# Kernel tuning notes

Hardware: AMD Instinct MI355X
Metric: run time of the kernel (lower is better)

Reference implementation:

```python
import jax, jax.numpy as jnp
import numpy as np
from jax import lax

DIM = 1024
HEADS = 16
KERNEL = 7
STRIDE = 4
EPS = 1e-5


def setup_inputs() -> dict:
    key = jax.random.key(0)
    ks = jax.random.split(key, 4)
    B, N = 2, 4096
    w_scale = 0.02
    return {
        "x": jax.random.normal(ks[0], (B, N, DIM), dtype=jnp.float32),
        "ln_w": jnp.ones((DIM,), jnp.float32),
        "ln_b": jnp.zeros((DIM,), jnp.float32),
        "Wk": jax.random.normal(ks[1], (DIM, DIM, KERNEL), dtype=jnp.float32) * w_scale,
        "Wv": jax.random.normal(ks[2], (DIM, DIM, KERNEL), dtype=jnp.float32) * w_scale,
        "Wq": jax.random.normal(ks[3], (DIM, DIM, KERNEL), dtype=jnp.float32) * w_scale,
    }


def _conv1d(x_bnd, w):
    # x: (B, N, D) -> conv over sequence dim with 'same' padding; w: (out_ch, in_ch, K)
    x_cn = jnp.transpose(x_bnd, (0, 2, 1))  # (B, D, N)
    pad = KERNEL // 2
    y = lax.conv_general_dilated(
        x_cn, w, window_strides=(1,), padding=[(pad, pad)],
        dimension_numbers=("NCH", "OIH", "NCH"))
    return jnp.transpose(y, (0, 2, 1))  # (B, N, D)


def reference(x, ln_w, ln_b, Wk, Wv, Wq):
    B, N, D = x.shape
    hd = D // HEADS
    # LayerNorm (biased variance, as in torch)
    mu = jnp.mean(x, axis=-1, keepdims=True)
    var = jnp.mean(jnp.square(x - mu), axis=-1, keepdims=True)
    x_n = (x - mu) / jnp.sqrt(var + EPS) * ln_w + ln_b

    K = _conv1d(x_n, Wk)                 # (B, N, D)
    V = _conv1d(x_n, Wv)                 # (B, N, D)
    Q = _conv1d(x_n, Wq)[:, ::STRIDE]    # (B, M, D) windowed queries
    M = Q.shape[1]

    Qh = Q.reshape(B, M, HEADS, hd).transpose(0, 2, 1, 3)  # (B, H, M, hd)
    Kh = K.reshape(B, N, HEADS, hd).transpose(0, 2, 1, 3)  # (B, H, N, hd)
    Vh = V.reshape(B, N, HEADS, hd).transpose(0, 2, 1, 3)  # (B, H, N, hd)

    scale = jnp.sqrt(jnp.asarray(hd, x.dtype))
    scores = jnp.einsum("bhmd,bhnd->bhmn", Qh, Kh) / scale  # (B, H, M, N)
    attn = jax.nn.softmax(scores, axis=-1)
    out = jnp.einsum("bhmn,bhnd->bhmd", attn, Vh)           # (B, H, M, hd)
    out = out.transpose(0, 2, 1, 3).reshape(B, M, D)
    return out + Q
```

## Files before the change

kernel.cpp:

```cpp
#include <hip/hip_runtime.h>

typedef __attribute__((ext_vector_type(4))) float f32x4;
typedef __attribute__((ext_vector_type(8))) short short8;
typedef __attribute__((ext_vector_type(4))) unsigned short u16x4;

#define AS1 __attribute__((address_space(1)))
#define AS3 __attribute__((address_space(3)))

__device__ __forceinline__ unsigned short f2bf(float f) {
  unsigned u = __float_as_uint(f);
  return (unsigned short)((u + 0x7FFFu + ((u >> 16) & 1u)) >> 16);
}
__device__ __forceinline__ unsigned short f2bf_fast(float f) {
  return (unsigned short)((__float_as_uint(f) + 0x8000u) >> 16);
}

__global__ __launch_bounds__(256) void ln_kernel(
    const float* __restrict__ x, const float* __restrict__ lw,
    const float* __restrict__ lb, unsigned short* __restrict__ xpad) {
  __shared__ float red[8];
  int row = blockIdx.x;
  int b = row >> 12, n = row & 4095;
  const float* xr = x + (size_t)row * 1024;
  int c = threadIdx.x * 4;
  f32x4 v = *(const f32x4*)(xr + c);
  float s = v[0] + v[1] + v[2] + v[3];
  float sq = v[0]*v[0] + v[1]*v[1] + v[2]*v[2] + v[3]*v[3];
#pragma unroll
  for (int off = 32; off; off >>= 1) {
    s  += __shfl_xor(s, off, 64);
    sq += __shfl_xor(sq, off, 64);
  }
  int w = threadIdx.x >> 6;
  if ((threadIdx.x & 63) == 0) { red[w*2] = s; red[w*2+1] = sq; }
  __syncthreads();
  float S  = red[0]+red[2]+red[4]+red[6];
  float SQ = red[1]+red[3]+red[5]+red[7];
  float mean = S * (1.0f/1024.0f);
  float var  = SQ * (1.0f/1024.0f) - mean*mean;
  float rstd = rsqrtf(var + 1e-5f);
  f32x4 wv = *(const f32x4*)(lw + c);
  f32x4 bv = *(const f32x4*)(lb + c);
  u16x4 o;
#pragma unroll
  for (int r = 0; r < 4; ++r) o[r] = f2bf((v[r]-mean)*rstd*wv[r] + bv[r]);
  *(u16x4*)(xpad + (((size_t)(b*4102 + n + 3)) << 10) + c) = o;
}

__global__ __launch_bounds__(256) void repack_kernel(
    const float* __restrict__ Wk, const float* __restrict__ Wv,
    const float* __restrict__ Wq, unsigned short* __restrict__ Wt) {
  __shared__ unsigned short t[7168];
  const float* W = (blockIdx.y == 0) ? Wk : (blockIdx.y == 1) ? Wv : Wq;
  int o = blockIdx.x;
  const float* row = W + (size_t)o * 7168;
  unsigned short* orow = Wt + ((size_t)(blockIdx.y * 1024 + o)) * 7168;
#pragma unroll
  for (int p = 0; p < 7; ++p) {
    int idx = p*1024 + threadIdx.x*4;
    f32x4 v = *(const f32x4*)(row + idx);
#pragma unroll
    for (int e = 0; e < 4; ++e) {
      unsigned j = idx + e;
      unsigned i = (j * 149797u) >> 20;
      unsigned k = j - i*7;
      t[k*1024 + i] = f2bf(v[e]);
    }
  }
  __syncthreads();
#pragma unroll
  for (int p = 0; p < 7; ++p) {
    int idx = p*1024 + threadIdx.x*4;
    *(u16x4*)(orow + idx) = *(const u16x4*)(t + idx);
  }
}

__global__ __launch_bounds__(512, 2) void conv256(
    const unsigned short* __restrict__ Apad,
    const unsigned short* __restrict__ Wt,
    unsigned short* __restrict__ Ksg, unsigned short* __restrict__ Vsg,
    float* __restrict__ Qp) {
  __shared__ unsigned short As[2][2][8192];
  __shared__ unsigned short Bs[2][2][8192];

  const int tid = threadIdx.x;
  const int w = tid >> 6, l = tid & 63;
  const int wm = w >> 2, wn = w & 3;
  const int l15 = l & 15, lh4 = l >> 4, l7 = l & 7;
  const int chA = ((l7 & 4) | (lh4 ^ (l7 & 3))) << 3;
  const int wOff = w << 9;
  const int bid = blockIdx.x;
  const int xcd = bid & 7, j = bid >> 3;
  const int ct = j & 7, rt = (xcd << 2) | (j >> 3);

  unsigned aOff[2][2], bOff[2][2];
#pragma unroll
  for (int i = 0; i < 2; ++i) {
    const int idx = i * 512 + tid;
    const int r = idx >> 3;
    const int clog8 = (((idx & 7) ^ (r & 7)) << 3);
#pragma unroll
    for (int hh = 0; hh < 2; ++hh) {
      const int rg = (rt << 8) + (hh << 7) + r;
      aOff[hh][i] = ((unsigned)((rg >> 12) * 4102 + (rg & 4095)) << 10) + clog8;
      const int cg = (ct << 8) + (hh << 7) + r;
      bOff[hh][i] = (unsigned)cg * 7168u + clog8;
    }
  }

  unsigned aRd[4], bRd[2];
#pragma unroll
  for (int fm = 0; fm < 4; ++fm)
    aRd[fm] = (unsigned)(((wm << 6) + (fm << 4) + l15) << 6) + chA;
#pragma unroll
  for (int fn = 0; fn < 2; ++fn)
    bRd[fn] = (unsigned)(((wn << 5) + (fn << 4) + l15) << 6) + chA;

  f32x4 acc[2][2][4][2] = {};
  short8 af[4][2], bfr[2][2];

#define STGA(BUF, HALF, T) do { \
    __builtin_amdgcn_global_load_lds((const AS1 void*)(Apad + aOff[HALF][0] + ((unsigned)(T) << 6)), (AS3 void*)&As[BUF][HALF][wOff], 16, 0, 0); \
    __builtin_amdgcn_global_load_lds((const AS1 void*)(Apad + aOff[HALF][1] + ((unsigned)(T) << 6)), (AS3 void*)&As[BUF][HALF][4096 + wOff], 16, 0, 0); \
  } while (0)
#define STGB(BUF, HALF, T) do { \
    __builtin_amdgcn_global_load_lds((const AS1 void*)(Wt + bOff[HALF][0] + ((unsigned)(T) << 6)), (AS3 void*)&Bs[BUF][HALF][wOff], 16, 0, 0); \
    __builtin_amdgcn_global_load_lds((const AS1 void*)(Wt + bOff[HALF][1] + ((unsigned)(T) << 6)), (AS3 void*)&Bs[BUF][HALF][4096 + wOff], 16, 0, 0); \
  } while (0)
#define LDA(BUF, MQ) do { \
    _Pragma("unroll") for (int fm = 0; fm < 4; ++fm) { \
      af[fm][0] = *(const short8*)&As[BUF][MQ][aRd[fm]]; \
      af[fm][1] = *(const short8*)&As[BUF][MQ][aRd[fm] ^ 32u]; } \
  } while (0)
#define LDB(BUF, NQ) do { \
    _Pragma("unroll") for (int fn = 0; fn < 2; ++fn) { \
      bfr[fn][0] = *(const short8*)&Bs[BUF][NQ][bRd[fn]]; \
      bfr[fn][1] = *(const short8*)&Bs[BUF][NQ][bRd[fn] ^ 32u]; } \
  } while (0)
#define MM(MQ, NQ) do { \
    _Pragma("unroll") for (int ks = 0; ks < 2; ++ks) \
    _Pragma("unroll") for (int fm = 0; fm < 4; ++fm) \
    _Pragma("unroll") for (int fn = 0; fn < 2; ++fn) \
      acc[MQ][NQ][fm][fn] = __builtin_amdgcn_mfma_f32_16x16x32_bf16(af[fm][ks], bfr[fn][ks], acc[MQ][NQ][fm][fn], 0, 0, 0); \
  } while (0)
#define BAR __builtin_amdgcn_s_barrier()
#define LGKM0 asm volatile("s_waitcnt lgkmcnt(0)" ::: "memory")
#define VM6 asm volatile("s_waitcnt vmcnt(6)" ::: "memory")
#define VM0 asm volatile("s_waitcnt vmcnt(0)" ::: "memory")
#define P1 __builtin_amdgcn_s_setprio(1)
#define P0 __builtin_amdgcn_s_setprio(0)

#define RUN_GEMM(NIT) do { \
    STGA(0, 0, 0); STGB(0, 0, 0); STGA(0, 1, 0); STGB(0, 1, 0); \
    STGA(1, 0, 1); STGB(1, 1, 1); STGA(1, 1, 1); \
    VM6; BAR; \
    for (int I = 0; I < (NIT) - 1; ++I) { \
      const int t0 = I * 2; \
      LDA(0, 0); LDB(0, 0); STGB(1, 0, t0 + 1); \
      BAR; LGKM0; P1; MM(0, 0); P0; BAR; \
      LDB(0, 1);            STGA(0, 0, t0 + 2); \
      BAR; LGKM0; P1; MM(0, 1); P0; BAR; \
      LDA(0, 1);            STGB(0, 1, t0 + 2); \
      BAR; LGKM0; P1; MM(1, 1); P0; BAR; \
      LDB(0, 0);            STGA(0, 1, t0 + 2); \
      BAR; LGKM0; P1; MM(1, 0); P0; VM6; BAR; \
      LDA(1, 0); LDB(1, 0); STGB(0, 0, t0 + 2); \
      BAR; LGKM0; P1; MM(0, 0); P0; BAR; \
      LDB(1, 1);            STGA(1, 0, t0 + 3); \
      BAR; LGKM0; P1; MM(0, 1); P0; BAR; \
      LDA(1, 1);            STGB(1, 1, t0 + 3); \
      BAR; LGKM0; P1; MM(1, 1); P0; BAR; \
      LDB(1, 0);            STGA(1, 1, t0 + 3); \
      BAR; LGKM0; P1; MM(1, 0); P0; VM6; BAR; \
    } \
    { \
      LDA(0, 0); LDB(0, 0); STGB(1, 0, ((NIT) - 1) * 2 + 1); \
      BAR; LGKM0; P1; MM(0, 0); P0; BAR; \
      LDB(0, 1); BAR; LGKM0; P1; MM(0, 1); P0; BAR; \
      LDA(0, 1); BAR; LGKM0; P1; MM(1, 1); P0; BAR; \
      LDB(0, 0); BAR; LGKM0; P1; MM(1, 0); P0; VM0; BAR; \
      LDA(1, 0); LDB(1, 0); BAR; LGKM0; P1; MM(0, 0); P0; BAR; \
      LDB(1, 1); BAR; LGKM0; P1; MM(0, 1); P0; BAR; \
      LDA(1, 1); BAR; LGKM0; P1; MM(1, 1); P0; BAR; \
      LDB(1, 0); BAR; LGKM0; P1; MM(1, 0); P0; BAR; \
    } \
  } while (0)

  RUN_GEMM(56);

  if (ct < 4) {
#pragma unroll
    for (int mq = 0; mq < 2; ++mq)
#pragma unroll
      for (int nq = 0; nq < 2; ++nq) {
        const int h = (ct << 2) + (nq << 1) + (wn >> 1);
        const int kd = wn & 1;
#pragma unroll
        for (int fm = 0; fm < 4; ++fm) {
          const int rbase = (rt << 8) + (mq << 7) + (wm << 6) + (fm << 4) + (lh4 << 2);
          const int b = rbase >> 12, n0 = rbase & 4095;
          const size_t base = ((((size_t)((b * 16 + h) * 2 + kd)) << 12) + n0) << 5;
#pragma unroll
          for (int fn = 0; fn < 2; ++fn) {
            const int d32 = (fn << 4) + l15;
#pragma unroll
            for (int rr = 0; rr < 4; ++rr)
              Ksg[base + ((size_t)rr << 5) + d32] = f2bf(acc[mq][nq][fm][fn][rr]);
          }
        }
      }
  } else {
#pragma unroll
    for (int mq = 0; mq < 2; ++mq)
#pragma unroll
      for (int nq = 0; nq < 2; ++nq) {
        const int h = ((ct - 4) << 2) + (nq << 1) + (wn >> 1);
        const int dhi = (wn & 1) << 5;
#pragma unroll
        for (int fm = 0; fm < 4; ++fm) {
          const int rbase = (rt << 8) + (mq << 7) + (wm << 6) + (fm << 4) + (lh4 << 2);
          const int b = rbase >> 12, n = rbase & 4095;
#pragma unroll
          for (int fn = 0; fn < 2; ++fn) {
            const int d = dhi + (fn << 4) + l15;
            const size_t rowbase =
                ((((((size_t)(b * 16 + h)) << 7) + (n >> 5)) << 6) + d) * 32 + (n & 31);
            u16x4 pv;
#pragma unroll
            for (int rr = 0; rr < 4; ++rr) pv[rr] = f2bf(acc[mq][nq][fm][fn][rr]);
            *(u16x4*)(Vsg + rowbase) = pv;
          }
        }
      }
  }

  const int qct = j & 3, qrt = j >> 2, kc = xcd;
  const unsigned kbase = (unsigned)kc * 896u;
#pragma unroll
  for (int i = 0; i < 2; ++i) {
    const int idx = i * 512 + tid;
    const int r = idx >> 3;
    const int clog8 = (((idx & 7) ^ (r & 7)) << 3);
#pragma unroll
    for (int hh = 0; hh < 2; ++hh) {
      const int rg = (qrt << 8) + (hh << 7) + r;
      aOff[hh][i] = ((unsigned)((rg >> 10) * 4102 + ((rg & 1023) << 2)) << 10) + clog8 + kbase;
      const int cg = 2048 + (qct << 8) + (hh << 7) + r;
      bOff[hh][i] = (unsigned)cg * 7168u + clog8 + kbase;
    }
  }
#pragma unroll
  for (int mq = 0; mq < 2; ++mq)
#pragma unroll
    for (int nq = 0; nq < 2; ++nq)
#pragma unroll
      for (int fm = 0; fm < 4; ++fm)
#pragma unroll
        for (int fn = 0; fn < 2; ++fn)
          acc[mq][nq][fm][fn] = (f32x4){0.f, 0.f, 0.f, 0.f};

  RUN_GEMM(7);

  float* Qc = Qp + ((size_t)kc << 21);
#pragma unroll
  for (int mq = 0; mq < 2; ++mq)
#pragma unroll
    for (int nq = 0; nq < 2; ++nq)
#pragma unroll
      for (int fm = 0; fm < 4; ++fm) {
        const int rq = (qrt << 8) + (mq << 7) + (wm << 6) + (fm << 4) + (lh4 << 2);
#pragma unroll
        for (int fn = 0; fn < 2; ++fn) {
          const int cq = (qct << 8) + (nq << 7) + (wn << 5) + (fn << 4) + l15;
#pragma unroll
          for (int rr = 0; rr < 4; ++rr)
            Qc[(((size_t)(rq + rr)) << 10) + cq] = acc[mq][nq][fm][fn][rr];
        }
      }
#undef STGA
#undef STGB
#undef LDA
#undef LDB
#undef MM
#undef BAR
#undef LGKM0
#undef VM6
#undef VM0
#undef P1
#undef P0
#undef RUN_GEMM
}

__global__ __launch_bounds__(256) void qfinal(
    const float* __restrict__ Qp, float* __restrict__ Qf,
    unsigned short* __restrict__ Qsg) {
  const int rq = blockIdx.x;
  const int b = rq >> 10, m = rq & 1023;
  const int c = threadIdx.x << 2;
  f32x4 v = {0.f, 0.f, 0.f, 0.f};
#pragma unroll
  for (int kc = 0; kc < 8; ++kc) {
    f32x4 p = *(const f32x4*)(Qp + ((size_t)kc << 21) + ((size_t)rq << 10) + c);
    v[0] += p[0]; v[1] += p[1]; v[2] += p[2]; v[3] += p[3];
  }
  *(f32x4*)(Qf + ((size_t)rq << 10) + c) = v;
  const int h = c >> 6, kd = (c >> 5) & 1, d32 = c & 31;
  u16x4 o;
#pragma unroll
  for (int e = 0; e < 4; ++e) o[e] = f2bf(v[e]);
  *(u16x4*)(Qsg + ((((size_t)((b * 16 + h) * 2 + kd)) << 10) + m) * 32 + d32) = o;
}

__global__ __launch_bounds__(512) void attn_kernel(
    const unsigned short* __restrict__ Ksg, const unsigned short* __restrict__ Vsg,
    const unsigned short* __restrict__ Qsg, const float* __restrict__ Qf,
    float* __restrict__ out) {
  __shared__ unsigned short Ks[2][8192];
  __shared__ unsigned short Vs[2][8192];
  __shared__ unsigned short Qs[8192];
  __shared__ unsigned short Ps[17408];
  const int tid = threadIdx.x, w = tid >> 6, l = tid & 63;
  const int g = blockIdx.x;
  const int bh = (g & 7) + (((g >> 3) & 3) << 3);
  const int qt = g >> 5;
  const int b = bh >> 4, h = bh & 15;
  const int m0 = qt << 7;
  const int quad = l >> 4, lc = l & 15, l3 = l & 3;
  const float C = 0.18033688011112042f;
  const int lsw = (l & 60) | ((l ^ (l >> 2)) & 3);

  const unsigned short* KgT = Ksg + ((size_t)bh << 18);
  const unsigned short* VgT = Vsg + ((size_t)bh << 18);
  const unsigned short* QgT = Qsg + ((size_t)bh << 16);

#pragma unroll
  for (int p = 0; p < 2; ++p) {
    int t = (w << 1) + p;
    int kd = t >> 3, ml = (t & 7) << 4;
    __builtin_amdgcn_global_load_lds(
        (const AS1 void*)(QgT + ((size_t)((kd << 10) + m0 + ml) << 5) + lsw*8),
        (AS3 void*)(Qs + (t << 9)), 16, 0, 0);
  }

#define STAGE_KV(BUF, N0) do { \
    _Pragma("unroll") for (int p = 0; p < 2; ++p) { \
      int t = (w << 1) + p; \
      __builtin_amdgcn_global_load_lds( \
          (const AS1 void*)(KgT + ((size_t)(((t >> 3) << 12) + (N0) + ((t & 7) << 4)) << 5) + lsw*8), \
          (AS3 void*)(Ks[BUF] + (t << 9)), 16, 0, 0); \
      __builtin_amdgcn_global_load_lds( \
          (const AS1 void*)(VgT + ((size_t)(((((N0) >> 5) + (t >> 2)) << 6) + ((t & 3) << 4)) << 5) + lsw*8), \
          (AS3 void*)(Vs[BUF] + (t << 9)), 16, 0, 0); \
    } \
  } while (0)

  float l_run = 0.f;
  f32x4 oacc[4] = {};
  unsigned short* Pw = Ps + w*2176;

  STAGE_KV(0, 0);
  asm volatile("s_waitcnt vmcnt(0)" ::: "memory");
  __builtin_amdgcn_s_barrier();

  for (int it = 0; it < 32; ++it) {
    const int cur = it & 1;
    if (it < 31) STAGE_KV(cur ^ 1, (it + 1) << 7);
    const unsigned short* Kc = Ks[cur];
    const unsigned short* Vc = Vs[cur];

    const int ch = (quad ^ l3) << 3;
    short8 ak[8][2];
#pragma unroll
    for (int k = 0; k < 2; ++k)
#pragma unroll
      for (int ni = 0; ni < 8; ++ni)
        ak[ni][k] = *(const short8*)(Kc + (k << 12) + ((ni<<4) + lc)*32 + ch);

    f32x4 sv[8] = {};
#pragma unroll
    for (int k = 0; k < 2; ++k) {
      short8 bq = *(const short8*)(Qs + (k << 12) + ((w<<4) + lc)*32 + ch);
#pragma unroll
      for (int ni = 0; ni < 8; ++ni)
        sv[ni] = __builtin_amdgcn_mfma_f32_16x16x32_bf16(ak[ni][k], bq, sv[ni], 0, 0, 0);
    }

    float su = 0.f;
#pragma unroll
    for (int ni = 0; ni < 8; ++ni) {
      u16x4 pv;
#pragma unroll
      for (int rr = 0; rr < 4; ++rr) {
        float pp = __builtin_amdgcn_exp2f(sv[ni][rr] * C);
        su += pp;
        pv[rr] = f2bf_fast(pp);
      }
      *(u16x4*)(Pw + lc*136 + (ni<<4) + (quad<<2)) = pv;
    }
    su += __shfl_xor(su, 16, 64);
    su += __shfl_xor(su, 32, 64);
    l_run += su;

#pragma unroll
    for (int kn = 0; kn < 4; ++kn) {
      short8 bp = *(const short8*)(Pw + lc*136 + (kn<<5) + (quad<<3));
#pragma unroll
      for (int dt = 0; dt < 4; ++dt) {
        short8 av = *(const short8*)(Vc + (kn << 11) + ((dt<<4) + lc)*32 + ch);
        oacc[dt] = __builtin_amdgcn_mfma_f32_16x16x32_bf16(av, bp, oacc[dt], 0, 0, 0);
      }
    }

    asm volatile("s_waitcnt vmcnt(0)" ::: "memory");
    __builtin_amdgcn_s_barrier();
  }
#undef STAGE_KV

  float invl = 1.0f / l_run;
  int m = m0 + (w<<4) + lc;
#pragma unroll
  for (int dt = 0; dt < 4; ++dt) {
    int d = (dt<<4) + (quad<<2);
    size_t off = (((size_t)(b << 10) + m) << 10) + (h << 6) + d;
    f32x4 qv = *(const f32x4*)(Qf + off);
    f32x4 ov;
#pragma unroll
    for (int rr = 0; rr < 4; ++rr) ov[rr] = oacc[dt][rr]*invl + qv[rr];
    *(f32x4*)(out + off) = ov;
  }
}

extern "C" void kernel_launch(void* const* d_in, const int* in_sizes, int n_in,
                              void* d_out, int out_size, void* d_ws, size_t ws_size,
                              hipStream_t stream) {
  const float* x  = (const float*)d_in[0];
  const float* lw = (const float*)d_in[1];
  const float* lb = (const float*)d_in[2];
  const float* Wk = (const float*)d_in[3];
  const float* Wv = (const float*)d_in[4];
  const float* Wq = (const float*)d_in[5];
  float* out = (float*)d_out;

  char* ws = (char*)d_ws;
  size_t off = 0;
  unsigned short* xpad = (unsigned short*)(ws + off); off += (size_t)2*4102*1024*2;
  unsigned short* Wt   = (unsigned short*)(ws + off); off += (size_t)3072*7168*2;
  unsigned short* Ksg  = (unsigned short*)(ws + off); off += (size_t)32*2*4096*32*2;
  unsigned short* Vsg  = (unsigned short*)(ws + off); off += (size_t)32*128*64*32*2;
  unsigned short* Qsg  = (unsigned short*)(ws + off); off += (size_t)32*2*1024*32*2;
  float*          Qf   = (float*)(ws + off);          off += (size_t)2048*1024*4;
  float*          Qp   = (float*)(ws + off);          off += (size_t)8*2048*1024*4;

  for (int b = 0; b < 2; ++b) {
    hipMemsetAsync(xpad + (size_t)b*4102*1024, 0, 3*1024*2, stream);
    hipMemsetAsync(xpad + ((size_t)b*4102 + 4099)*1024, 0, 3*1024*2, stream);
  }
  ln_kernel<<<dim3(8192), dim3(256), 0, stream>>>(x, lw, lb, xpad);
  repack_kernel<<<dim3(1024, 3), dim3(256), 0, stream>>>(Wk, Wv, Wq, Wt);
  conv256<<<dim3(256), dim3(512), 0, stream>>>(xpad, Wt, Ksg, Vsg, Qp);
  qfinal<<<dim3(2048), dim3(256), 0, stream>>>(Qp, Qf, Qsg);
  attn_kernel<<<dim3(256), dim3(512), 0, stream>>>(Ksg, Vsg, Qsg, Qf, out);
}
```

Before: 479.8 us.

## Double-buffer MFMA register fragments to overlap LDS reads with matrix math

The main conv-GEMM loop now keeps two register slots for the A and B fragments. The LDS reads for the next sub-tile are issued before the MFMAs of the current one, so each phase uses one barrier instead of two. The wait counts on the global-to-LDS loads are retuned to vmcnt(4), and the order of the initial staging loads is swapped to match. This is meant to hide LDS read latency and barrier cost behind MFMA work, at the price of more VGPRs and some risk of races from the fewer barriers.

```diff
diff --git a/kernel.cpp b/kernel.cpp
--- a/kernel.cpp
+++ b/kernel.cpp
@@ -117,7 +117,7 @@
     bRd[fn] = (unsigned)(((wn << 5) + (fn << 4) + l15) << 6) + chA;
 
   f32x4 acc[2][2][4][2] = {};
-  short8 af[4][2], bfr[2][2];
+  short8 afS[2][4][2], bfS[2][2][2];
 
 #define STGA(BUF, HALF, T) do { \
     __builtin_amdgcn_global_load_lds((const AS1 void*)(Apad + aOff[HALF][0] + ((unsigned)(T) << 6)), (AS3 void*)&As[BUF][HALF][wOff], 16, 0, 0); \
@@ -127,62 +127,55 @@
     __builtin_amdgcn_global_load_lds((const AS1 void*)(Wt + bOff[HALF][0] + ((unsigned)(T) << 6)), (AS3 void*)&Bs[BUF][HALF][wOff], 16, 0, 0); \
     __builtin_amdgcn_global_load_lds((const AS1 void*)(Wt + bOff[HALF][1] + ((unsigned)(T) << 6)), (AS3 void*)&Bs[BUF][HALF][4096 + wOff], 16, 0, 0); \
   } while (0)
-#define LDA(BUF, MQ) do { \
+#define LDAs(S, BUF, MQ) do { \
     _Pragma("unroll") for (int fm = 0; fm < 4; ++fm) { \
-      af[fm][0] = *(const short8*)&As[BUF][MQ][aRd[fm]]; \
-      af[fm][1] = *(const short8*)&As[BUF][MQ][aRd[fm] ^ 32u]; } \
-  } while (0)
-#define LDB(BUF, NQ) do { \
+      afS[S][fm][0] = *(const short8*)&As[BUF][MQ][aRd[fm]]; \
+      afS[S][fm][1] = *(const short8*)&As[BUF][MQ][aRd[fm] ^ 32u]; } \
+  } while (0)
+#define LDBs(S, BUF, NQ) do { \
     _Pragma("unroll") for (int fn = 0; fn < 2; ++fn) { \
-      bfr[fn][0] = *(const short8*)&Bs[BUF][NQ][bRd[fn]]; \
-      bfr[fn][1] = *(const short8*)&Bs[BUF][NQ][bRd[fn] ^ 32u]; } \
-  } while (0)
-#define MM(MQ, NQ) do { \
+      bfS[S][fn][0] = *(const short8*)&Bs[BUF][NQ][bRd[fn]]; \
+      bfS[S][fn][1] = *(const short8*)&Bs[BUF][NQ][bRd[fn] ^ 32u]; } \
+  } while (0)
+#define MMs(SA, SB, MQ, NQ) do { \
     _Pragma("unroll") for (int ks = 0; ks < 2; ++ks) \
     _Pragma("unroll") for (int fm = 0; fm < 4; ++fm) \
     _Pragma("unroll") for (int fn = 0; fn < 2; ++fn) \
-      acc[MQ][NQ][fm][fn] = __builtin_amdgcn_mfma_f32_16x16x32_bf16(af[fm][ks], bfr[fn][ks], acc[MQ][NQ][fm][fn], 0, 0, 0); \
+      acc[MQ][NQ][fm][fn] = __builtin_amdgcn_mfma_f32_16x16x32_bf16(afS[SA][fm][ks], bfS[SB][fn][ks], acc[MQ][NQ][fm][fn], 0, 0, 0); \
   } while (0)
 #define BAR __builtin_amdgcn_s_barrier()
 #define LGKM0 asm volatile("s_waitcnt lgkmcnt(0)" ::: "memory")
 #define VM6 asm volatile("s_waitcnt vmcnt(6)" ::: "memory")
+#define VM4 asm volatile("s_waitcnt vmcnt(4)" ::: "memory")
 #define VM0 asm volatile("s_waitcnt vmcnt(0)" ::: "memory")
 #define P1 __builtin_amdgcn_s_setprio(1)
 #define P0 __builtin_amdgcn_s_setprio(0)
 
 #define RUN_GEMM(NIT) do { \
-    STGA(0, 0, 0); STGB(0, 0, 0); STGA(0, 1, 0); STGB(0, 1, 0); \
+    STGA(0, 0, 0); STGB(0, 0, 0); STGB(0, 1, 0); STGA(0, 1, 0); \
     STGA(1, 0, 1); STGB(1, 1, 1); STGA(1, 1, 1); \
     VM6; BAR; \
+    LDAs(0, 0, 0); LDBs(0, 0, 0); \
     for (int I = 0; I < (NIT) - 1; ++I) { \
       const int t0 = I * 2; \
-      LDA(0, 0); LDB(0, 0); STGB(1, 0, t0 + 1); \
-      BAR; LGKM0; P1; MM(0, 0); P0; BAR; \
-      LDB(0, 1);            STGA(0, 0, t0 + 2); \
-      BAR; LGKM0; P1; MM(0, 1); P0; BAR; \
-      LDA(0, 1);            STGB(0, 1, t0 + 2); \
-      BAR; LGKM0; P1; MM(1, 1); P0; BAR; \
-      LDB(0, 0);            STGA(0, 1, t0 + 2); \
-      BAR; LGKM0; P1; MM(1, 0); P0; VM6; BAR; \
-      LDA(1, 0); LDB(1, 0); STGB(0, 0, t0 + 2); \
-      BAR; LGKM0; P1; MM(0, 0); P0; BAR; \
-      LDB(1, 1);            STGA(1, 0, t0 + 3); \
-      BAR; LGKM0; P1; MM(0, 1); P0; BAR; \
-      LDA(1, 1);            STGB(1, 1, t0 + 3); \
-      BAR; LGKM0; P1; MM(1, 1); P0; BAR; \
-      LDB(1, 0);            STGA(1, 1, t0 + 3); \
-      BAR; LGKM0; P1; MM(1, 0); P0; VM6; BAR; \
+      BAR; LGKM0; LDBs(1, 0, 1);                STGB(1, 0, t0 + 1); P1; MMs(0, 0, 0, 0); P0; \
+      BAR; LGKM0; LDAs(1, 0, 1);                STGA(0, 0, t0 + 2); P1; MMs(0, 1, 0, 1); P0; \
+      BAR; LGKM0;                               STGB(0, 1, t0 + 2); P1; MMs(1, 1, 1, 1); P0; VM4; \
+      BAR; LGKM0; LDAs(0, 1, 0); LDBs(1, 1, 0); STGA(0, 1, t0 + 2); P1; MMs(1, 0, 1, 0); P0; \
+      BAR; LGKM0; LDBs(0, 1, 1);                STGB(0, 0, t0 + 2); P1; MMs(0, 1, 0, 0); P0; \
+      BAR; LGKM0; LDAs(1, 1, 1);                STGA(1, 0, t0 + 3); P1; MMs(0, 0, 0, 1); P0; \
+      BAR; LGKM0;                               STGB(1, 1, t0 + 3); P1; MMs(1, 0, 1, 1); P0; VM4; \
+      BAR; LGKM0; LDAs(0, 0, 0); LDBs(0, 0, 0); STGA(1, 1, t0 + 3); P1; MMs(1, 1, 1, 0); P0; \
     } \
     { \
-      LDA(0, 0); LDB(0, 0); STGB(1, 0, ((NIT) - 1) * 2 + 1); \
-      BAR; LGKM0; P1; MM(0, 0); P0; BAR; \
-      LDB(0, 1); BAR; LGKM0; P1; MM(0, 1); P0; BAR; \
-      LDA(0, 1); BAR; LGKM0; P1; MM(1, 1); P0; BAR; \
-      LDB(0, 0); BAR; LGKM0; P1; MM(1, 0); P0; VM0; BAR; \
-      LDA(1, 0); LDB(1, 0); BAR; LGKM0; P1; MM(0, 0); P0; BAR; \
-      LDB(1, 1); BAR; LGKM0; P1; MM(0, 1); P0; BAR; \
-      LDA(1, 1); BAR; LGKM0; P1; MM(1, 1); P0; BAR; \
-      LDB(1, 0); BAR; LGKM0; P1; MM(1, 0); P0; BAR; \
+      BAR; LGKM0; LDBs(1, 0, 1); STGB(1, 0, 2*(NIT) - 1); P1; MMs(0, 0, 0, 0); P0; \
+      BAR; LGKM0; LDAs(1, 0, 1);                          P1; MMs(0, 1, 0, 1); P0; \
+      BAR; LGKM0;                                         P1; MMs(1, 1, 1, 1); P0; VM0; \
+      BAR; LGKM0; LDAs(0, 1, 0); LDBs(1, 1, 0);           P1; MMs(1, 0, 1, 0); P0; \
+      BAR; LGKM0; LDBs(0, 1, 1);                          P1; MMs(0, 1, 0, 0); P0; \
+      BAR; LGKM0; LDAs(1, 1, 1);                          P1; MMs(0, 0, 0, 1); P0; \
+      BAR; LGKM0;                                         P1; MMs(1, 0, 1, 1); P0; \
+      BAR; LGKM0;                                         P1; MMs(1, 1, 1, 0); P0; \
     } \
   } while (0)
 
@@ -279,12 +272,13 @@
       }
 #undef STGA
 #undef STGB
-#undef LDA
-#undef LDB
-#undef MM
+#undef LDAs
+#undef LDBs
+#undef MMs
 #undef BAR
 #undef LGKM0
 #undef VM6
+#undef VM4
 #undef VM0
 #undef P1
 #undef P0
```

Measured after the change: 534.5 us. +11.4%, slower.
